# Kernel tuning notes

Hardware: AMD Instinct MI355X
Metric: run time of the kernel (lower is better)

Reference implementation:

```python
import jax, jax.numpy as jnp
import numpy as np


def setup_inputs() -> dict:
    key = jax.random.key(0)
    k1, k2, k3 = jax.random.split(key, 3)
    B, R, N, A, U = 64, 5, 512, 64, 128
    adjacency = jax.random.uniform(k1, (B, R, N, N), dtype=jnp.float32)
    features = jax.random.normal(k2, (B, N, A), dtype=jnp.float32)
    kernel = jax.random.normal(k3, (R, A, U), dtype=jnp.float32) * 0.05
    bias = jnp.zeros((R, 1, U), dtype=jnp.float32)
    return {"adjacency": adjacency, "features": features, "kernel": kernel, "bias": bias}


def reference(adjacency, features, kernel, bias):
    # adjacency: [B, R, N, N], features: [B, N, A]
    # aggregate neighbourhoods per relation: [B, R, N, A]
    agg = jnp.einsum("brnm,bma->brna", adjacency, features)
    # relation-wise projection: [B, R, N, U]
    dp = jnp.einsum("brna,rau->brnu", agg, kernel) + bias  # bias broadcasts over B, N
    # sum over relation axis, then activation: [B, N, U]
    return jax.nn.relu(jnp.sum(dp, axis=1))
```

## Files before the change

### kernel.cpp

```cpp
#include <hip/hip_runtime.h>
#include <hip/hip_bf16.h>

typedef __attribute__((ext_vector_type(4))) float f32x4;
typedef __attribute__((ext_vector_type(8))) short s16x8;
typedef __attribute__((ext_vector_type(4))) short s16x4;

__device__ __forceinline__ unsigned short f2bf(float f) {
  __hip_bfloat16 h = __float2bfloat16(f);
  return __builtin_bit_cast(unsigned short, h);
}

__global__ void k_ft(const float* __restrict__ F, unsigned short* __restrict__ FT) {
  __shared__ float t[64][65];
  const int b  = blockIdx.x >> 3;
  const int m0 = (blockIdx.x & 7) * 64;
  const int tid = threadIdx.x;
  {
    const int row = tid >> 2, ac = (tid & 3) * 16;
    const float* src = F + ((size_t)b * 512 + m0 + row) * 64 + ac;
    #pragma unroll
    for (int j = 0; j < 4; ++j) {
      f32x4 v = *(const f32x4*)(src + j * 4);
      t[row][ac + j * 4 + 0] = v[0]; t[row][ac + j * 4 + 1] = v[1];
      t[row][ac + j * 4 + 2] = v[2]; t[row][ac + j * 4 + 3] = v[3];
    }
  }
  __syncthreads();
  {
    const int a = tid >> 2, mc = (tid & 3) * 16;
    unsigned short* dst = FT + ((size_t)b * 64 + a) * 512 + m0 + mc;
    s16x8 p0, p1;
    #pragma unroll
    for (int j = 0; j < 8; ++j) {
      p0[j] = (short)f2bf(t[mc + j][a]);
      p1[j] = (short)f2bf(t[mc + 8 + j][a]);
    }
    *(s16x8*)(dst) = p0;
    *(s16x8*)(dst + 8) = p1;
  }
}

__global__ void k_kt(const float* __restrict__ K, const float* __restrict__ bias,
                     unsigned short* __restrict__ KT, float* __restrict__ bsum) {
  const int gtid = threadIdx.x + blockIdx.x * blockDim.x;
  for (int idx = gtid; idx < 128 * 320; idx += blockDim.x * gridDim.x) {
    const int u = idx / 320, ra = idx % 320;
    KT[idx] = f2bf(K[(size_t)ra * 128 + u]);
  }
  if (gtid < 128) {
    float s = 0.f;
    #pragma unroll
    for (int r = 0; r < 5; ++r) s += bias[r * 128 + gtid];
    bsum[gtid] = s;
  }
}

__global__ __launch_bounds__(256, 3) void k_fused(const float* __restrict__ Adj,
                                                  const unsigned short* __restrict__ FT,
                                                  const unsigned short* __restrict__ KT,
                                                  const float* __restrict__ bsum,
                                                  float* __restrict__ out) {
  __shared__ unsigned short ag[64][328];
  const int b  = blockIdx.x >> 3;
  const int nt = blockIdx.x & 7;
  const int w  = threadIdx.x >> 6;
  const int l  = threadIdx.x & 63;
  const int l15 = l & 15, g = l >> 4;
  const int n = nt * 64 + w * 16 + l15;

  const float* adjRow = Adj + (size_t)(b * 5) * 262144 + (size_t)n * 512 + g * 8;
  const unsigned short* ftp = FT + ((size_t)b * 64 + l15) * 512 + g * 8;

  f32x4 acc[5][4];
  #pragma unroll
  for (int r = 0; r < 5; ++r)
    #pragma unroll
    for (int at = 0; at < 4; ++at) acc[r][at] = (f32x4)0.f;

  #pragma unroll 2
  for (int ks = 0; ks < 16; ++ks) {
    s16x8 ffrag[4];
    #pragma unroll
    for (int at = 0; at < 4; ++at)
      ffrag[at] = *(const s16x8*)(ftp + at * 16 * 512 + ks * 32);
    #pragma unroll
    for (int r = 0; r < 5; ++r) {
      const float* ap = adjRow + (size_t)r * 262144 + ks * 32;
      f32x4 a0 = *(const f32x4*)(ap);
      f32x4 a1 = *(const f32x4*)(ap + 4);
      s16x8 bfrag;
      #pragma unroll
      for (int j = 0; j < 4; ++j) {
        bfrag[j]     = (short)f2bf(a0[j]);
        bfrag[4 + j] = (short)f2bf(a1[j]);
      }
      #pragma unroll
      for (int at = 0; at < 4; ++at)
        acc[r][at] = __builtin_amdgcn_mfma_f32_16x16x32_bf16(ffrag[at], bfrag, acc[r][at], 0, 0, 0);
    }
  }

  #pragma unroll
  for (int r = 0; r < 5; ++r)
    #pragma unroll
    for (int at = 0; at < 4; ++at) {
      s16x4 pk;
      pk[0] = (short)f2bf(acc[r][at][0]); pk[1] = (short)f2bf(acc[r][at][1]);
      pk[2] = (short)f2bf(acc[r][at][2]); pk[3] = (short)f2bf(acc[r][at][3]);
      *(s16x4*)&ag[w * 16 + l15][r * 64 + at * 16 + g * 4] = pk;
    }
  __syncthreads();

  const unsigned short* kp = KT + (size_t)l15 * 320 + g * 8;
  f32x4 o[8];
  #pragma unroll
  for (int ut = 0; ut < 8; ++ut) o[ut] = (f32x4)0.f;

  #pragma unroll 2
  for (int ks = 0; ks < 10; ++ks) {
    s16x8 af = *(const s16x8*)&ag[w * 16 + l15][ks * 32 + g * 8];
    #pragma unroll
    for (int ut = 0; ut < 8; ++ut) {
      s16x8 bfr = *(const s16x8*)(kp + (size_t)ut * 16 * 320 + ks * 32);
      o[ut] = __builtin_amdgcn_mfma_f32_16x16x32_bf16(af, bfr, o[ut], 0, 0, 0);
    }
  }

  #pragma unroll
  for (int ut = 0; ut < 8; ++ut) {
    const int u = ut * 16 + l15;
    const float bs = bsum[u];
    float* op = out + ((size_t)(b * 512 + nt * 64 + w * 16 + g * 4)) * 128 + u;
    #pragma unroll
    for (int t = 0; t < 4; ++t) {
      float vv = o[ut][t] + bs;
      op[(size_t)t * 128] = vv > 0.f ? vv : 0.f;
    }
  }
}

extern "C" void kernel_launch(void* const* d_in, const int* in_sizes, int n_in,
                              void* d_out, int out_size, void* d_ws, size_t ws_size,
                              hipStream_t stream) {
  const float* adj  = (const float*)d_in[0];
  const float* feat = (const float*)d_in[1];
  const float* kern = (const float*)d_in[2];
  const float* bias = (const float*)d_in[3];
  float* out = (float*)d_out;

  char* ws = (char*)d_ws;
  unsigned short* FT   = (unsigned short*)ws;
  unsigned short* KT   = (unsigned short*)(ws + 4194304);
  float*          bsum = (float*)(ws + 4194304 + 81920);

  hipLaunchKernelGGL(k_ft,    dim3(512), dim3(256), 0, stream, feat, FT);
  hipLaunchKernelGGL(k_kt,    dim3(160), dim3(256), 0, stream, kern, bias, KT, bsum);
  hipLaunchKernelGGL(k_fused, dim3(512), dim3(256), 0, stream, adj, FT, KT, bsum, out);
  (void)in_sizes; (void)n_in; (void)out_size; (void)ws_size;
}
```

Baseline: 101.4 us.

## Stream adjacency through double-buffered LDS and fuse per-relation projection via shuffles

The fused kernel now loads adjacency tiles with coalesced row-contiguous 128-column loads into a per-wave double-buffered LDS region, prefetching the next chunk into registers while the current one is consumed. After each relation's aggregation, results are converted to bf16 and rearranged with cross-lane shuffles straight into MFMA A-fragments, so the projection is accumulated per relation. This removes the shared aggregation buffer and the block barrier. It cuts live accumulators from 20 to 4 vectors but lowers launch-bounds occupancy from 3 to 2 blocks and adds LDS traffic plus shuffle work.

```diff
diff --git a/kernel.cpp b/kernel.cpp
--- a/kernel.cpp
+++ b/kernel.cpp
@@ -3,7 +3,7 @@
 
 typedef __attribute__((ext_vector_type(4))) float f32x4;
 typedef __attribute__((ext_vector_type(8))) short s16x8;
-typedef __attribute__((ext_vector_type(4))) short s16x4;
+typedef __attribute__((ext_vector_type(4))) int i32x4;
 
 __device__ __forceinline__ unsigned short f2bf(float f) {
   __hip_bfloat16 h = __float2bfloat16(f);
@@ -55,74 +55,107 @@
   }
 }
 
-__global__ __launch_bounds__(256, 3) void k_fused(const float* __restrict__ Adj,
+__global__ __launch_bounds__(256, 2) void k_fused(const float* __restrict__ Adj,
                                                   const unsigned short* __restrict__ FT,
                                                   const unsigned short* __restrict__ KT,
                                                   const float* __restrict__ bsum,
                                                   float* __restrict__ out) {
-  __shared__ unsigned short ag[64][328];
+  __shared__ float lds[2][4][16][128];
   const int b  = blockIdx.x >> 3;
   const int nt = blockIdx.x & 7;
   const int w  = threadIdx.x >> 6;
   const int l  = threadIdx.x & 63;
   const int l15 = l & 15, g = l >> 4;
-  const int n = nt * 64 + w * 16 + l15;
 
-  const float* adjRow = Adj + (size_t)(b * 5) * 262144 + (size_t)n * 512 + g * 8;
-  const unsigned short* ftp = FT + ((size_t)b * 64 + l15) * 512 + g * 8;
+  const float* adjW = Adj + (size_t)b * 5 * 262144 + (size_t)(nt * 64 + w * 16) * 512;
+  const int srow = l >> 5;
+  const int scol = (l & 31) * 4;
 
-  f32x4 acc[5][4];
+  f32x4 G[8];
   #pragma unroll
-  for (int r = 0; r < 5; ++r)
+  for (int i = 0; i < 8; ++i)
+    G[i] = *(const f32x4*)(adjW + (size_t)(i * 2 + srow) * 512 + scol);
+  #pragma unroll
+  for (int i = 0; i < 8; ++i)
+    *(f32x4*)&lds[0][w][i * 2 + srow][scol] = G[i];
+
+  f32x4 out_acc[8];
+  #pragma unroll
+  for (int u = 0; u < 8; ++u) out_acc[u] = (f32x4)0.f;
+  f32x4 acc[4];
+  #pragma unroll
+  for (int at = 0; at < 4; ++at) acc[at] = (f32x4)0.f;
+
+  const unsigned short* ftW = FT + (size_t)b * 64 * 512;
+
+  #pragma unroll
+  for (int s = 0; s < 20; ++s) {
+    const int r = s >> 2, mc = s & 3;
+    const int buf = s & 1;
+
+    if (s < 19) {
+      const int r1 = (s + 1) >> 2, mc1 = (s + 1) & 3;
+      const float* p = adjW + (size_t)r1 * 262144 + mc1 * 128;
+      #pragma unroll
+      for (int i = 0; i < 8; ++i)
+        G[i] = *(const f32x4*)(p + (size_t)(i * 2 + srow) * 512 + scol);
+    }
+
     #pragma unroll
-    for (int at = 0; at < 4; ++at) acc[r][at] = (f32x4)0.f;
-
-  #pragma unroll 2
-  for (int ks = 0; ks < 16; ++ks) {
-    s16x8 ffrag[4];
-    #pragma unroll
-    for (int at = 0; at < 4; ++at)
-      ffrag[at] = *(const s16x8*)(ftp + at * 16 * 512 + ks * 32);
-    #pragma unroll
-    for (int r = 0; r < 5; ++r) {
-      const float* ap = adjRow + (size_t)r * 262144 + ks * 32;
-      f32x4 a0 = *(const f32x4*)(ap);
-      f32x4 a1 = *(const f32x4*)(ap + 4);
+    for (int ksl = 0; ksl < 4; ++ksl) {
+      const int m = mc * 128 + ksl * 32 + g * 8;
+      f32x4 lo = *(const f32x4*)&lds[buf][w][l15][ksl * 32 + g * 8];
+      f32x4 hi = *(const f32x4*)&lds[buf][w][l15][ksl * 32 + g * 8 + 4];
       s16x8 bfrag;
       #pragma unroll
       for (int j = 0; j < 4; ++j) {
-        bfrag[j]     = (short)f2bf(a0[j]);
-        bfrag[4 + j] = (short)f2bf(a1[j]);
+        bfrag[j]     = (short)f2bf(lo[j]);
+        bfrag[4 + j] = (short)f2bf(hi[j]);
       }
       #pragma unroll
-      for (int at = 0; at < 4; ++at)
-        acc[r][at] = __builtin_amdgcn_mfma_f32_16x16x32_bf16(ffrag[at], bfrag, acc[r][at], 0, 0, 0);
+      for (int at = 0; at < 4; ++at) {
+        s16x8 ff = *(const s16x8*)(ftW + (size_t)(at * 16 + l15) * 512 + m);
+        acc[at] = __builtin_amdgcn_mfma_f32_16x16x32_bf16(ff, bfrag, acc[at], 0, 0, 0);
+      }
     }
-  }
 
-  #pragma unroll
-  for (int r = 0; r < 5; ++r)
-    #pragma unroll
-    for (int at = 0; at < 4; ++at) {
-      s16x4 pk;
-      pk[0] = (short)f2bf(acc[r][at][0]); pk[1] = (short)f2bf(acc[r][at][1]);
-      pk[2] = (short)f2bf(acc[r][at][2]); pk[3] = (short)f2bf(acc[r][at][3]);
-      *(s16x4*)&ag[w * 16 + l15][r * 64 + at * 16 + g * 4] = pk;
+    if (mc == 3) {
+      int pk0[4], pk1[4];
+      #pragma unroll
+      for (int at = 0; at < 4; ++at) {
+        pk0[at] = (int)((unsigned)f2bf(acc[at][0]) | ((unsigned)f2bf(acc[at][1]) << 16));
+        pk1[at] = (int)((unsigned)f2bf(acc[at][2]) | ((unsigned)f2bf(acc[at][3]) << 16));
+      }
+      const int sel = g >> 1;
+      const int sl0 = ((g & 1) * 2) * 16 + l15;
+      const int sl1 = sl0 + 16;
+      #pragma unroll
+      for (int ks2 = 0; ks2 < 2; ++ks2) {
+        const int at0 = ks2 * 2, at1 = at0 + 1;
+        int j0a = __shfl(pk0[at0], sl0), j0b = __shfl(pk0[at1], sl0);
+        int j1a = __shfl(pk1[at0], sl0), j1b = __shfl(pk1[at1], sl0);
+        int j2a = __shfl(pk0[at0], sl1), j2b = __shfl(pk0[at1], sl1);
+        int j3a = __shfl(pk1[at0], sl1), j3b = __shfl(pk1[at1], sl1);
+        i32x4 afi;
+        afi[0] = sel ? j0b : j0a;
+        afi[1] = sel ? j1b : j1a;
+        afi[2] = sel ? j2b : j2a;
+        afi[3] = sel ? j3b : j3a;
+        s16x8 af = __builtin_bit_cast(s16x8, afi);
+        #pragma unroll
+        for (int ut = 0; ut < 8; ++ut) {
+          s16x8 kf = *(const s16x8*)(KT + (size_t)(ut * 16 + l15) * 320 + r * 64 + ks2 * 32 + g * 8);
+          out_acc[ut] = __builtin_amdgcn_mfma_f32_16x16x32_bf16(af, kf, out_acc[ut], 0, 0, 0);
+        }
+      }
+      #pragma unroll
+      for (int at = 0; at < 4; ++at) acc[at] = (f32x4)0.f;
     }
-  __syncthreads();
 
-  const unsigned short* kp = KT + (size_t)l15 * 320 + g * 8;
-  f32x4 o[8];
-  #pragma unroll
-  for (int ut = 0; ut < 8; ++ut) o[ut] = (f32x4)0.f;
-
-  #pragma unroll 2
-  for (int ks = 0; ks < 10; ++ks) {
-    s16x8 af = *(const s16x8*)&ag[w * 16 + l15][ks * 32 + g * 8];
-    #pragma unroll
-    for (int ut = 0; ut < 8; ++ut) {
-      s16x8 bfr = *(const s16x8*)(kp + (size_t)ut * 16 * 320 + ks * 32);
-      o[ut] = __builtin_amdgcn_mfma_f32_16x16x32_bf16(af, bfr, o[ut], 0, 0, 0);
+    if (s < 19) {
+      #pragma unroll
+      for (int i = 0; i < 8; ++i)
+        *(f32x4*)&lds[buf ^ 1][w][i * 2 + srow][scol] = G[i];
     }
   }
 
@@ -130,10 +163,10 @@
   for (int ut = 0; ut < 8; ++ut) {
     const int u = ut * 16 + l15;
     const float bs = bsum[u];
-    float* op = out + ((size_t)(b * 512 + nt * 64 + w * 16 + g * 4)) * 128 + u;
+    float* op = out + ((size_t)b * 512 + nt * 64 + w * 16 + g * 4) * 128 + u;
     #pragma unroll
     for (int t = 0; t < 4; ++t) {
-      float vv = o[ut][t] + bs;
+      float vv = out_acc[ut][t] + bs;
       op[(size_t)t * 128] = vv > 0.f ? vv : 0.f;
     }
   }
```

After: 151.9 us. +49.8%, slower.

## Stage adjacency tiles through per-wave double-buffered LDS with register prefetch

Applied to the files above, without the earlier changes.

Each wave now loads its 16x128 adjacency tile with coalesced row-wise float4 loads, converts it to bf16 and stores it into a per-wave double-buffered LDS tile. The next relation/K-chunk is prefetched into registers while MFMAs run on the current buffer. The K-loop is restructured into 128-wide chunks with features fragments hoisted per chunk. Because LDS is private to each wave, the block-wide barrier before the projection is removed. The costs are higher register pressure (launch bounds lowered to 2 blocks per CU) and more LDS traffic. Correctness relies on wave-local ordering of the LDS writes and reads, since no explicit wave barrier is issued.

```diff
diff --git a/kernel.cpp b/kernel.cpp
--- a/kernel.cpp
+++ b/kernel.cpp
@@ -55,21 +55,38 @@
   }
 }
 
-__global__ __launch_bounds__(256, 3) void k_fused(const float* __restrict__ Adj,
+__global__ __launch_bounds__(256, 2) void k_fused(const float* __restrict__ Adj,
                                                   const unsigned short* __restrict__ FT,
                                                   const unsigned short* __restrict__ KT,
                                                   const float* __restrict__ bsum,
                                                   float* __restrict__ out) {
-  __shared__ unsigned short ag[64][328];
+  __shared__ unsigned short q[4][2][16][136];
+  __shared__ unsigned short ag[4][16][328];
   const int b  = blockIdx.x >> 3;
   const int nt = blockIdx.x & 7;
   const int w  = threadIdx.x >> 6;
   const int l  = threadIdx.x & 63;
   const int l15 = l & 15, g = l >> 4;
-  const int n = nt * 64 + w * 16 + l15;
 
-  const float* adjRow = Adj + (size_t)(b * 5) * 262144 + (size_t)n * 512 + g * 8;
-  const unsigned short* ftp = FT + ((size_t)b * 64 + l15) * 512 + g * 8;
+  const float* adjW = Adj + (size_t)b * 5 * 262144 + (size_t)(nt * 64 + w * 16) * 512;
+  const unsigned short* ftW = FT + (size_t)b * 64 * 512;
+  const int srow = l >> 5;
+  const int scol = (l & 31) * 4;
+
+  unsigned short (*Q)[16][136] = q[w];
+  unsigned short (*agw)[328] = ag[w];
+
+  f32x4 G[8];
+  #pragma unroll
+  for (int i = 0; i < 8; ++i)
+    G[i] = *(const f32x4*)(adjW + (size_t)(i * 2 + srow) * 512 + scol);
+  #pragma unroll
+  for (int i = 0; i < 8; ++i) {
+    s16x4 pk;
+    pk[0] = (short)f2bf(G[i][0]); pk[1] = (short)f2bf(G[i][1]);
+    pk[2] = (short)f2bf(G[i][2]); pk[3] = (short)f2bf(G[i][3]);
+    *(s16x4*)&Q[0][i * 2 + srow][scol] = pk;
+  }
 
   f32x4 acc[5][4];
   #pragma unroll
@@ -77,26 +94,46 @@
     #pragma unroll
     for (int at = 0; at < 4; ++at) acc[r][at] = (f32x4)0.f;
 
-  #pragma unroll 2
-  for (int ks = 0; ks < 16; ++ks) {
-    s16x8 ffrag[4];
+  int cur = 0;
+  for (int ks4 = 0; ks4 < 4; ++ks4) {
+    s16x8 ffrag[4][4];
     #pragma unroll
-    for (int at = 0; at < 4; ++at)
-      ffrag[at] = *(const s16x8*)(ftp + at * 16 * 512 + ks * 32);
+    for (int ksl = 0; ksl < 4; ++ksl)
+      #pragma unroll
+      for (int at = 0; at < 4; ++at)
+        ffrag[ksl][at] = *(const s16x8*)(ftW + (size_t)(at * 16 + l15) * 512 + ks4 * 128 + ksl * 32 + g * 8);
+
     #pragma unroll
     for (int r = 0; r < 5; ++r) {
-      const float* ap = adjRow + (size_t)r * 262144 + ks * 32;
-      f32x4 a0 = *(const f32x4*)(ap);
-      f32x4 a1 = *(const f32x4*)(ap + 4);
-      s16x8 bfrag;
+      const bool have_next = (r < 4) || (ks4 < 3);
+      if (have_next) {
+        const int rn = (r == 4) ? 0 : r + 1;
+        const int kn = (r == 4) ? ks4 + 1 : ks4;
+        const float* p = adjW + (size_t)rn * 262144 + (size_t)kn * 128;
+        #pragma unroll
+        for (int i = 0; i < 8; ++i)
+          G[i] = *(const f32x4*)(p + (size_t)(i * 2 + srow) * 512 + scol);
+      }
+
       #pragma unroll
-      for (int j = 0; j < 4; ++j) {
-        bfrag[j]     = (short)f2bf(a0[j]);
-        bfrag[4 + j] = (short)f2bf(a1[j]);
+      for (int ksl = 0; ksl < 4; ++ksl) {
+        s16x8 bfrag = *(const s16x8*)&Q[cur][l15][ksl * 32 + g * 8];
+        acc[r][0] = __builtin_amdgcn_mfma_f32_16x16x32_bf16(ffrag[ksl][0], bfrag, acc[r][0], 0, 0, 0);
+        acc[r][1] = __builtin_amdgcn_mfma_f32_16x16x32_bf16(ffrag[ksl][1], bfrag, acc[r][1], 0, 0, 0);
+        acc[r][2] = __builtin_amdgcn_mfma_f32_16x16x32_bf16(ffrag[ksl][2], bfrag, acc[r][2], 0, 0, 0);
+        acc[r][3] = __builtin_amdgcn_mfma_f32_16x16x32_bf16(ffrag[ksl][3], bfrag, acc[r][3], 0, 0, 0);
       }
-      #pragma unroll
-      for (int at = 0; at < 4; ++at)
-        acc[r][at] = __builtin_amdgcn_mfma_f32_16x16x32_bf16(ffrag[at], bfrag, acc[r][at], 0, 0, 0);
+
+      if (have_next) {
+        #pragma unroll
+        for (int i = 0; i < 8; ++i) {
+          s16x4 pk;
+          pk[0] = (short)f2bf(G[i][0]); pk[1] = (short)f2bf(G[i][1]);
+          pk[2] = (short)f2bf(G[i][2]); pk[3] = (short)f2bf(G[i][3]);
+          *(s16x4*)&Q[cur ^ 1][i * 2 + srow][scol] = pk;
+        }
+        cur ^= 1;
+      }
     }
   }
 
@@ -107,22 +144,20 @@
       s16x4 pk;
       pk[0] = (short)f2bf(acc[r][at][0]); pk[1] = (short)f2bf(acc[r][at][1]);
       pk[2] = (short)f2bf(acc[r][at][2]); pk[3] = (short)f2bf(acc[r][at][3]);
-      *(s16x4*)&ag[w * 16 + l15][r * 64 + at * 16 + g * 4] = pk;
+      *(s16x4*)&agw[l15][r * 64 + at * 16 + g * 4] = pk;
     }
-  __syncthreads();
 
-  const unsigned short* kp = KT + (size_t)l15 * 320 + g * 8;
   f32x4 o[8];
   #pragma unroll
   for (int ut = 0; ut < 8; ++ut) o[ut] = (f32x4)0.f;
 
   #pragma unroll 2
   for (int ks = 0; ks < 10; ++ks) {
-    s16x8 af = *(const s16x8*)&ag[w * 16 + l15][ks * 32 + g * 8];
+    s16x8 af = *(const s16x8*)&agw[l15][ks * 32 + g * 8];
     #pragma unroll
     for (int ut = 0; ut < 8; ++ut) {
-      s16x8 bfr = *(const s16x8*)(kp + (size_t)ut * 16 * 320 + ks * 32);
-      o[ut] = __builtin_amdgcn_mfma_f32_16x16x32_bf16(af, bfr, o[ut], 0, 0, 0);
+      s16x8 kf = *(const s16x8*)(KT + (size_t)(ut * 16 + l15) * 320 + ks * 32 + g * 8);
+      o[ut] = __builtin_amdgcn_mfma_f32_16x16x32_bf16(af, kf, o[ut], 0, 0, 0);
     }
   }
 
@@ -130,7 +165,7 @@
   for (int ut = 0; ut < 8; ++ut) {
     const int u = ut * 16 + l15;
     const float bs = bsum[u];
-    float* op = out + ((size_t)(b * 512 + nt * 64 + w * 16 + g * 4)) * 128 + u;
+    float* op = out + ((size_t)b * 512 + nt * 64 + w * 16 + g * 4) * 128 + u;
     #pragma unroll
     for (int t = 0; t < 4; ++t) {
       float vv = o[ut][t] + bs;
```

New measurement: 97.42 us. 4.0% less time.

## Prefetch adjacency fragments one step ahead and drop block barrier in fused kernel

Applied to the files above, without the earlier changes.

Software-pipelines the adjacency loads in the first GEMM: the next k-step's fp32 fragments for all five relations are loaded into registers while the current ones are converted and fed to MFMA. The shared staging buffer is split per wave so the block-wide __syncthreads can be removed, each wave reusing only its own rows. Block indices are remapped to interleave batches across consecutive blocks, and launch bounds drop occupancy from 3 to 2 blocks per CU to make room for the extra prefetch registers. The trade-off is fewer resident waves for latency hiding in exchange for explicit prefetching.

```diff
diff --git a/kernel.cpp b/kernel.cpp
--- a/kernel.cpp
+++ b/kernel.cpp
@@ -55,21 +55,31 @@
   }
 }
 
-__global__ __launch_bounds__(256, 3) void k_fused(const float* __restrict__ Adj,
+__global__ __launch_bounds__(256, 2) void k_fused(const float* __restrict__ Adj,
                                                   const unsigned short* __restrict__ FT,
                                                   const unsigned short* __restrict__ KT,
                                                   const float* __restrict__ bsum,
                                                   float* __restrict__ out) {
-  __shared__ unsigned short ag[64][328];
-  const int b  = blockIdx.x >> 3;
-  const int nt = blockIdx.x & 7;
+  __shared__ unsigned short ag[4][16][328];
+  const int bi = blockIdx.x;
+  const int L  = (bi & 7) * 64 + (bi >> 3);
+  const int b  = L >> 3;
+  const int nt = L & 7;
   const int w  = threadIdx.x >> 6;
   const int l  = threadIdx.x & 63;
   const int l15 = l & 15, g = l >> 4;
   const int n = nt * 64 + w * 16 + l15;
 
-  const float* adjRow = Adj + (size_t)(b * 5) * 262144 + (size_t)n * 512 + g * 8;
+  const float* adjL = Adj + (size_t)b * 5 * 262144 + (size_t)n * 512 + g * 8;
   const unsigned short* ftp = FT + ((size_t)b * 64 + l15) * 512 + g * 8;
+
+  f32x4 G[5][2];
+  #pragma unroll
+  for (int r = 0; r < 5; ++r) {
+    const float* p = adjL + (size_t)r * 262144;
+    G[r][0] = *(const f32x4*)(p);
+    G[r][1] = *(const f32x4*)(p + 4);
+  }
 
   f32x4 acc[5][4];
   #pragma unroll
@@ -77,29 +87,31 @@
     #pragma unroll
     for (int at = 0; at < 4; ++at) acc[r][at] = (f32x4)0.f;
 
-  #pragma unroll 2
   for (int ks = 0; ks < 16; ++ks) {
     s16x8 ffrag[4];
     #pragma unroll
     for (int at = 0; at < 4; ++at)
-      ffrag[at] = *(const s16x8*)(ftp + at * 16 * 512 + ks * 32);
+      ffrag[at] = *(const s16x8*)(ftp + (size_t)at * 16 * 512 + ks * 32);
+    const int kn = (ks < 15) ? ks + 1 : 15;
     #pragma unroll
     for (int r = 0; r < 5; ++r) {
-      const float* ap = adjRow + (size_t)r * 262144 + ks * 32;
-      f32x4 a0 = *(const f32x4*)(ap);
-      f32x4 a1 = *(const f32x4*)(ap + 4);
       s16x8 bfrag;
       #pragma unroll
       for (int j = 0; j < 4; ++j) {
-        bfrag[j]     = (short)f2bf(a0[j]);
-        bfrag[4 + j] = (short)f2bf(a1[j]);
+        bfrag[j]     = (short)f2bf(G[r][0][j]);
+        bfrag[4 + j] = (short)f2bf(G[r][1][j]);
       }
-      #pragma unroll
-      for (int at = 0; at < 4; ++at)
-        acc[r][at] = __builtin_amdgcn_mfma_f32_16x16x32_bf16(ffrag[at], bfrag, acc[r][at], 0, 0, 0);
+      const float* p = adjL + (size_t)r * 262144 + kn * 32;
+      G[r][0] = *(const f32x4*)(p);
+      G[r][1] = *(const f32x4*)(p + 4);
+      acc[r][0] = __builtin_amdgcn_mfma_f32_16x16x32_bf16(ffrag[0], bfrag, acc[r][0], 0, 0, 0);
+      acc[r][1] = __builtin_amdgcn_mfma_f32_16x16x32_bf16(ffrag[1], bfrag, acc[r][1], 0, 0, 0);
+      acc[r][2] = __builtin_amdgcn_mfma_f32_16x16x32_bf16(ffrag[2], bfrag, acc[r][2], 0, 0, 0);
+      acc[r][3] = __builtin_amdgcn_mfma_f32_16x16x32_bf16(ffrag[3], bfrag, acc[r][3], 0, 0, 0);
     }
   }
 
+  unsigned short (*agw)[328] = ag[w];
   #pragma unroll
   for (int r = 0; r < 5; ++r)
     #pragma unroll
@@ -107,22 +119,20 @@
       s16x4 pk;
       pk[0] = (short)f2bf(acc[r][at][0]); pk[1] = (short)f2bf(acc[r][at][1]);
       pk[2] = (short)f2bf(acc[r][at][2]); pk[3] = (short)f2bf(acc[r][at][3]);
-      *(s16x4*)&ag[w * 16 + l15][r * 64 + at * 16 + g * 4] = pk;
+      *(s16x4*)&agw[l15][r * 64 + at * 16 + g * 4] = pk;
     }
-  __syncthreads();
 
-  const unsigned short* kp = KT + (size_t)l15 * 320 + g * 8;
   f32x4 o[8];
   #pragma unroll
   for (int ut = 0; ut < 8; ++ut) o[ut] = (f32x4)0.f;
 
   #pragma unroll 2
   for (int ks = 0; ks < 10; ++ks) {
-    s16x8 af = *(const s16x8*)&ag[w * 16 + l15][ks * 32 + g * 8];
+    s16x8 af = *(const s16x8*)&agw[l15][ks * 32 + g * 8];
     #pragma unroll
     for (int ut = 0; ut < 8; ++ut) {
-      s16x8 bfr = *(const s16x8*)(kp + (size_t)ut * 16 * 320 + ks * 32);
-      o[ut] = __builtin_amdgcn_mfma_f32_16x16x32_bf16(af, bfr, o[ut], 0, 0, 0);
+      s16x8 kf = *(const s16x8*)(KT + (size_t)(ut * 16 + l15) * 320 + ks * 32 + g * 8);
+      o[ut] = __builtin_amdgcn_mfma_f32_16x16x32_bf16(af, kf, o[ut], 0, 0, 0);
     }
   }
 
@@ -130,7 +140,7 @@
   for (int ut = 0; ut < 8; ++ut) {
     const int u = ut * 16 + l15;
     const float bs = bsum[u];
-    float* op = out + ((size_t)(b * 512 + nt * 64 + w * 16 + g * 4)) * 128 + u;
+    float* op = out + ((size_t)b * 512 + nt * 64 + w * 16 + g * 4) * 128 + u;
     #pragma unroll
     for (int t = 0; t < 4; ++t) {
       float vv = o[ut][t] + bs;
```

Result: slower. 103.6 us (+2.2%).
